# Kernel tuning notes

Measured on AMD Instinct MI355X. Metric: run time of the kernel, lower is better.

The kernel has to match this reference:

```python
import jax, jax.numpy as jnp
import numpy as np

DEPTH = 6
INPUT_DIM = 512
HIDDEN = [128, 64]
OUT_DIM = 8
BATCH = 8192
NUM_LEAVES = 2 ** DEPTH            # 64
NUM_INTERNAL = 2 ** DEPTH - 1      # 63 routing Dense(1, sigmoid) nodes


def setup_inputs() -> dict:
    key = jax.random.key(0)
    ks = jax.random.split(key, 9)
    s = lambda fan_in: 1.0 / np.sqrt(fan_in)
    return {
        "x": jax.random.normal(ks[0], (BATCH, INPUT_DIM), dtype=jnp.float32),
        # routers: one Dense(input_dim -> 1) per internal node
        "router_W": jax.random.normal(ks[1], (NUM_INTERNAL, INPUT_DIM), dtype=jnp.float32) * s(INPUT_DIM),
        "router_b": jnp.zeros((NUM_INTERNAL,), dtype=jnp.float32),
        # leaf MLPs: Dense(512->128, relu) -> Dense(128->64, relu) -> Dense(64->8, linear), one per leaf
        "W1": jax.random.normal(ks[2], (NUM_LEAVES, INPUT_DIM, HIDDEN[0]), dtype=jnp.float32) * s(INPUT_DIM),
        "b1": jnp.zeros((NUM_LEAVES, HIDDEN[0]), dtype=jnp.float32),
        "W2": jax.random.normal(ks[3], (NUM_LEAVES, HIDDEN[0], HIDDEN[1]), dtype=jnp.float32) * s(HIDDEN[0]),
        "b2": jnp.zeros((NUM_LEAVES, HIDDEN[1]), dtype=jnp.float32),
        "W3": jax.random.normal(ks[4], (NUM_LEAVES, HIDDEN[1], OUT_DIM), dtype=jnp.float32) * s(HIDDEN[1]),
        "b3": jnp.zeros((NUM_LEAVES, OUT_DIM), dtype=jnp.float32),
    }


def reference(x, router_W, router_b, W1, b1, W2, b2, W3, b3):
    B = x.shape[0]
    depth = int(np.log2(router_W.shape[0] + 1))
    # All routing probabilities in one fused GEMM: [B, num_internal]
    route = jax.nn.sigmoid(jnp.einsum('bi,ni->bn', x, router_W) + router_b)
    # Soft routing down the tree: interleave left/right child probabilities per level.
    p = jnp.ones((B, 1), dtype=x.dtype)
    offset = 0
    for level in range(depth):  # small fixed loop over tree levels
        n = 2 ** level
        d = route[:, offset:offset + n]              # P(go left) at each node in level
        p = jnp.stack([p * d, p * (1.0 - d)], axis=-1).reshape(B, 2 * n)
        offset += n
    # p: [B, num_leaves] leaf arrival probabilities (sums to 1 per row)
    # Leaf experts as batched (grouped) GEMMs over the leaf axis l.
    h = jax.nn.relu(jnp.einsum('bi,lih->blh', x, W1) + b1)   # [B, L, 128]
    h = jax.nn.relu(jnp.einsum('blh,lhk->blk', h, W2) + b2)  # [B, L, 64]
    pred = jnp.einsum('blk,lko->blo', h, W3) + b3            # [B, L, out] (linear output act)
    # Weighted mixture over leaves.
    return jnp.einsum('bl,blo->bo', p, pred)                 # [B, out]
```

## Files before the change

### kernel.cpp

```cpp
#include <hip/hip_runtime.h>
#include <hip/hip_bf16.h>


typedef _Float16 f16;
typedef _Float16 f16x8 __attribute__((ext_vector_type(8)));
typedef float    f32x4 __attribute__((ext_vector_type(4)));
typedef float    f32x16 __attribute__((ext_vector_type(16)));

#define MFMA16(a,b,c) __builtin_amdgcn_mfma_f32_16x16x32_f16((a),(b),(c),0,0,0)
#define MFMA32(a,b,c) __builtin_amdgcn_mfma_f32_32x32x16_f16((a),(b),(c),0,0,0)

typedef const __attribute__((address_space(1))) void gv_t;
typedef __attribute__((address_space(3))) void lv_t;
__device__ __forceinline__ void cp16(const void* g, char* lds_dst) {
  __builtin_amdgcn_global_load_lds((gv_t*)g, (lv_t*)lds_dst, 16, 0, 0);
}

#define WS_XH    0u
#define WS_W1F   8388608u
#define WS_W2F   16777216u
#define WS_W3F   17825792u
#define WS_RWF   17956864u
#define WS_NEED  18022400u

#define L_X   0
#define L_H1  32768
#define L_H2  41472
#define L_P   46080
#define L_TOT 50176

__global__ __launch_bounds__(256) void prep_all(
    const float* __restrict__ x, const float* __restrict__ rW,
    const float* __restrict__ W1, const float* __restrict__ W2,
    const float* __restrict__ W3,
    f16* __restrict__ xh, f16* __restrict__ w1f, f16* __restrict__ w2f,
    f16* __restrict__ w3f, f16* __restrict__ rwf) {
  __shared__ float sb[8704];
  const int bid = blockIdx.x, t = threadIdx.x;
  if (bid < 512) {
    const int l = bid >> 3, kc = bid & 7;
    const float* src = W1 + ((size_t)l * 512 + kc * 64) * 128;
#pragma unroll
    for (int i = 0; i < 32; ++i) {
      int idx = t + i * 256;
      int k_l = idx >> 7, n = idx & 127;
      sb[n * 68 + k_l] = src[(size_t)k_l * 128 + n];
    }
    __syncthreads();
#pragma unroll
    for (int p = 0; p < 4; ++p) {
      int c = p * 4 + (t >> 6);
      int ng = c >> 2, ksl = c & 3;
      int lane = t & 63;
      int n = ng * 32 + (lane & 31);
      int k0 = ksl * 16 + (lane >> 5) * 8;
      f16x8 h;
#pragma unroll
      for (int j = 0; j < 8; ++j) h[j] = (f16)sb[n * 68 + k0 + j];
      *(f16x8*)(w1f + ((size_t)((l * 4 + ng) * 32 + kc * 4 + ksl) * 64 + lane) * 8) = h;
    }
  } else if (bid < 768) {
    size_t base = (size_t)(bid - 512) * 16384;
#pragma unroll
    for (int i = 0; i < 8; ++i) {
      size_t idx = base + ((size_t)t + i * 256) * 8;
      float4 a = *(const float4*)(x + idx);
      float4 b = *(const float4*)(x + idx + 4);
      f16x8 h = {(f16)a.x,(f16)a.y,(f16)a.z,(f16)a.w,(f16)b.x,(f16)b.y,(f16)b.z,(f16)b.w};
      *(f16x8*)(xh + idx) = h;
    }
  } else if (bid < 832) {
    const int l = bid - 768;
    const float* src = W2 + (size_t)l * 128 * 64;
#pragma unroll
    for (int i = 0; i < 32; ++i) {
      int idx = t + i * 256;
      int k_l = idx >> 6, n = idx & 63;
      sb[n * 132 + k_l] = src[(size_t)k_l * 64 + n];
    }
    __syncthreads();
#pragma unroll
    for (int p = 0; p < 4; ++p) {
      int c = p * 4 + (t >> 6);
      int nb = c >> 2, ks = c & 3;
      int lane = t & 63;
      int n = nb * 16 + (lane & 15);
      int k0 = ks * 32 + (lane >> 4) * 8;
      f16x8 h;
#pragma unroll
      for (int j = 0; j < 8; ++j) h[j] = (f16)sb[n * 132 + k0 + j];
      *(f16x8*)(w2f + ((size_t)((l * 4 + nb) * 4 + ks) * 64 + lane) * 8) = h;
    }
    if (t < 128) {
      int ks = t >> 6, lane = t & 63;
      int n = lane & 15;
      int k0 = ks * 32 + (lane >> 4) * 8;
      f16x8 h;
#pragma unroll
      for (int j = 0; j < 8; ++j)
        h[j] = (n < 8) ? (f16)W3[((size_t)l * 64 + k0 + j) * 8 + n] : (f16)0.f;
      *(f16x8*)(w3f + ((size_t)(l * 2 + ks) * 64 + lane) * 8) = h;
    }
  } else {
    int c = (bid - 832) * 4 + (t >> 6);
    int ngr = c >> 5, ks = c & 31;
    int lane = t & 63;
    int n = ngr * 32 + (lane & 31);
    int k0 = ks * 16 + (lane >> 5) * 8;
    f16x8 h;
#pragma unroll
    for (int j = 0; j < 8; ++j)
      h[j] = (n < 63) ? (f16)rW[(size_t)n * 512 + k0 + j] : (f16)0.f;
    *(f16x8*)(rwf + ((size_t)c * 64 + lane) * 8) = h;
  }
}

__global__ __launch_bounds__(256, 2) void fused_tree(
    const f16* __restrict__ xh, const f16* __restrict__ w1f,
    const f16* __restrict__ w2f, const f16* __restrict__ w3f,
    const f16* __restrict__ rwf, const float* __restrict__ rb,
    const float* __restrict__ b1, const float* __restrict__ b2,
    const float* __restrict__ b3, float* __restrict__ out) {
  __shared__ char smem[L_TOT];
  f16*   x_lds   = (f16*)(smem + L_X);
  f16*   h1_lds  = (f16*)(smem + L_H1);
  float* route_s = (float*)(smem + L_H1);
  f16*   h2_lds  = (f16*)(smem + L_H2);
  float* p_lds   = (float*)(smem + L_P);

  const int t = threadIdx.x;
  const int w = t >> 6, L = t & 63;
  const int l16 = L & 15, quad = L >> 4;
  const int r31 = L & 31, kp = L >> 5;

  const int bid = blockIdx.x;
  const int r8 = bid & 7;
  const int lg0 = (r8 >> 1) * 16;
  const int btp = (bid >> 3) * 2 + (r8 & 1);
  const int b0 = btp * 64;

#pragma unroll
  for (int j = 0; j < 8; ++j) {
    int r = w * 8 + j;
    int u = (L & 56) | ((L & 7) ^ (r & 7));
    cp16(xh + (size_t)(b0 + 32 + r) * 512 + u * 8, smem + r * 1024);
  }
  f16x8 a0[32];
#pragma unroll
  for (int ks = 0; ks < 32; ++ks)
    a0[ks] = *(const f16x8*)(xh + (size_t)(b0 + r31) * 512 + ks * 16 + kp * 8);
  __syncthreads();

  {
    const int btr = w >> 1, ngr = w & 1;
    f32x16 accr;
#pragma unroll
    for (int i = 0; i < 16; ++i) accr[i] = 0.f;
    const f16* rbase = rwf + (size_t)(ngr * 32) * 512 + (size_t)L * 8;
#pragma unroll
    for (int ks = 0; ks < 32; ++ks) {
      f16x8 B = *(const f16x8*)(rbase + (size_t)ks * 512);
      f16x8 A;
      if (btr == 0) A = a0[ks];
      else {
        int u = ks * 2 + kp;
        A = *(const f16x8*)(x_lds + r31 * 512 + ((u & 56) | ((u & 7) ^ (r31 & 7))) * 8);
      }
      accr = MFMA32(A, B, accr);
    }
    int node = ngr * 32 + r31;
    float rbv = (node < 63) ? rb[node] : 0.f;
#pragma unroll
    for (int reg = 0; reg < 16; ++reg) {
      int rr = btr * 32 + (reg & 3) + 8 * (reg >> 2) + 4 * kp;
      route_s[rr * 68 + node] = 1.f / (1.f + __expf(-(accr[reg] + rbv)));
    }
  }
  __syncthreads();
  float prod[4];
  {
    int row = t >> 2, j0 = t & 3;
#pragma unroll
    for (int i = 0; i < 4; ++i) {
      int l = lg0 + j0 * 4 + i;
      float pr = 1.f;
#pragma unroll
      for (int lev = 0; lev < 6; ++lev) {
        int node = (1 << lev) - 1 + (l >> (6 - lev));
        float d = route_s[row * 68 + node];
        pr *= ((l >> (5 - lev)) & 1) ? (1.f - d) : d;
      }
      prod[i] = pr;
    }
  }
  __syncthreads();
  {
    int row = t >> 2, j0 = t & 3;
#pragma unroll
    for (int i = 0; i < 4; ++i) p_lds[row * 16 + j0 * 4 + i] = prod[i];
  }
  __syncthreads();

  const f16* w1base = w1f + ((size_t)(lg0 * 4 + w) * 32) * 512 + (size_t)L * 8;
  f16x8 bq[2][4];
#pragma unroll
  for (int s = 0; s < 4; ++s) bq[0][s] = *(const f16x8*)(w1base + (size_t)s * 512);

  f32x4 acc_out = {0.f, 0.f, 0.f, 0.f};
  const int mt = w >> 1, nt2 = w & 1;

#pragma unroll 1
  for (int li = 0; li < 16; ++li) {
    const int l = lg0 + li;
    const size_t leafoff = (size_t)li * 65536;

    f32x16 acc1r, acc1l;
#pragma unroll
    for (int i = 0; i < 16; ++i) { acc1r[i] = 0.f; acc1l[i] = 0.f; }

#pragma unroll
    for (int q = 0; q < 8; ++q) {
      f16x8 A1[4];
#pragma unroll
      for (int s = 0; s < 4; ++s) {
        int u = (q * 4 + s) * 2 + kp;
        A1[s] = *(const f16x8*)(x_lds + r31 * 512 + ((u & 56) | ((u & 7) ^ (r31 & 7))) * 8);
      }
      size_t nxt = (q < 7) ? (leafoff + (size_t)(q + 1) * 2048)
                           : ((li < 15) ? (leafoff + 65536) : (leafoff + 7 * 2048));
#pragma unroll
      for (int s = 0; s < 4; ++s)
        bq[(q + 1) & 1][s] = *(const f16x8*)(w1base + nxt + (size_t)s * 512);
#pragma unroll
      for (int s = 0; s < 4; ++s)
        acc1r = MFMA32(a0[q * 4 + s], bq[q & 1][s], acc1r);
#pragma unroll
      for (int s = 0; s < 4; ++s)
        acc1l = MFMA32(A1[s], bq[q & 1][s], acc1l);
    }

    f16x8 bw2[2][4];
#pragma unroll
    for (int n16 = 0; n16 < 2; ++n16)
#pragma unroll
      for (int ks = 0; ks < 4; ++ks)
        bw2[n16][ks] = *(const f16x8*)(w2f + ((size_t)((l * 4 + nt2 * 2 + n16) * 4 + ks) * 64 + L) * 8);
    f16x8 bw3[2];
#pragma unroll
    for (int ks = 0; ks < 2; ++ks)
      bw3[ks] = *(const f16x8*)(w3f + ((size_t)(l * 2 + ks) * 64 + L) * 8);

    const int n1 = w * 32 + r31;
    const float bias1 = b1[l * 128 + n1];

#pragma unroll
    for (int reg = 0; reg < 16; ++reg) {
      int rr = (reg & 3) + 8 * (reg >> 2) + 4 * kp;
      float v = acc1r[reg] + bias1;
      h1_lds[rr * 136 + n1] = (f16)(v > 0.f ? v : 0.f);
    }
    __syncthreads();

#define GEMM2_BT(btv)                                                          \
    {                                                                          \
      f32x4 acc2[2] = {{0.f,0.f,0.f,0.f},{0.f,0.f,0.f,0.f}};                   \
      _Pragma("unroll")                                                        \
      for (int ks = 0; ks < 4; ++ks) {                                         \
        f16x8 A = *(const f16x8*)(h1_lds + (mt * 16 + l16) * 136 + ks * 32 + quad * 8); \
        _Pragma("unroll")                                                      \
        for (int n16 = 0; n16 < 2; ++n16) acc2[n16] = MFMA16(A, bw2[n16][ks], acc2[n16]); \
      }                                                                        \
      _Pragma("unroll")                                                        \
      for (int n16 = 0; n16 < 2; ++n16) {                                      \
        int n2 = nt2 * 32 + n16 * 16 + l16;                                    \
        float bias2 = b2[l * 64 + n2];                                         \
        _Pragma("unroll")                                                      \
        for (int rg = 0; rg < 4; ++rg) {                                       \
          int r2 = mt * 16 + quad * 4 + rg;                                    \
          float v = acc2[n16][rg] + bias2;                                     \
          v = v > 0.f ? v : 0.f;                                               \
          h2_lds[r2 * 72 + n2] = (f16)(v * p_lds[((btv) * 32 + r2) * 16 + li]); \
        }                                                                      \
      }                                                                        \
    }

    GEMM2_BT(0)
    __syncthreads();

    if (w < 2) {
#pragma unroll
      for (int ks = 0; ks < 2; ++ks) {
        f16x8 A = *(const f16x8*)(h2_lds + ((w & 1) * 16 + l16) * 72 + ks * 32 + quad * 8);
        acc_out = MFMA16(A, bw3[ks], acc_out);
      }
    }
#pragma unroll
    for (int reg = 0; reg < 16; ++reg) {
      int rr = (reg & 3) + 8 * (reg >> 2) + 4 * kp;
      float v = acc1l[reg] + bias1;
      h1_lds[rr * 136 + n1] = (f16)(v > 0.f ? v : 0.f);
    }
    __syncthreads();

    GEMM2_BT(1)
    __syncthreads();

    if (w >= 2) {
#pragma unroll
      for (int ks = 0; ks < 2; ++ks) {
        f16x8 A = *(const f16x8*)(h2_lds + ((w & 1) * 16 + l16) * 72 + ks * 32 + quad * 8);
        acc_out = MFMA16(A, bw3[ks], acc_out);
      }
    }
#undef GEMM2_BT
  }

  if (l16 < 8) {
    const int btf = w >> 1, mtf = w & 1;
    float b3v[16];
#pragma unroll
    for (int li2 = 0; li2 < 16; ++li2) b3v[li2] = b3[(lg0 + li2) * 8 + l16];
#pragma unroll
    for (int rg = 0; rg < 4; ++rg) {
      int rloc = btf * 32 + mtf * 16 + quad * 4 + rg;
      float v = acc_out[rg];
#pragma unroll
      for (int li2 = 0; li2 < 16; ++li2) v += p_lds[rloc * 16 + li2] * b3v[li2];
      atomicAdd(out + (size_t)(b0 + rloc) * 8 + l16, v);
    }
  }
}

extern "C" void kernel_launch(void* const* d_in, const int* in_sizes, int n_in,
                              void* d_out, int out_size, void* d_ws, size_t ws_size,
                              hipStream_t stream) {
  const float* x  = (const float*)d_in[0];
  const float* rW = (const float*)d_in[1];
  const float* rb = (const float*)d_in[2];
  const float* W1 = (const float*)d_in[3];
  const float* b1 = (const float*)d_in[4];
  const float* W2 = (const float*)d_in[5];
  const float* b2 = (const float*)d_in[6];
  const float* W3 = (const float*)d_in[7];
  const float* b3 = (const float*)d_in[8];
  float* out = (float*)d_out;

  if (ws_size < WS_NEED) return;

  char* ws = (char*)d_ws;
  f16* xh  = (f16*)(ws + WS_XH);
  f16* w1f = (f16*)(ws + WS_W1F);
  f16* w2f = (f16*)(ws + WS_W2F);
  f16* w3f = (f16*)(ws + WS_W3F);
  f16* rwf = (f16*)(ws + WS_RWF);

  hipMemsetAsync(d_out, 0, (size_t)out_size * sizeof(float), stream);
  prep_all<<<848, 256, 0, stream>>>(x, rW, W1, W2, W3, xh, w1f, w2f, w3f, rwf);
  fused_tree<<<512, 256, 0, stream>>>(xh, w1f, w2f, w3f, rwf, rb, b1, b2, b3, out);
}
```

Baseline: 198.2 us.

## Software-pipeline leaf GEMM1 with GEMM2/GEMM3 and double-size h1/h2 buffers

Restructures the per-leaf loop so the layer-1 GEMM for the next leaf is interleaved with the layer-2 and layer-3 work of the current leaf. The h1 and h2 LDS buffers are enlarged to hold both 32-row batch halves at once, which cuts the syncthreads per leaf from four to two. Routing-probability values are preloaded into registers, one barrier in the prologue is removed, and LDS pads in prep and route are changed to odd strides to reduce bank conflicts. The cost is more LDS per block and higher register pressure from the live accumulators, which may lower occupancy.

```diff
diff --git a/kernel.cpp b/kernel.cpp
--- a/kernel.cpp
+++ b/kernel.cpp
@@ -25,9 +25,9 @@
 
 #define L_X   0
 #define L_H1  32768
-#define L_H2  41472
-#define L_P   46080
-#define L_TOT 50176
+#define L_H2  50176
+#define L_P   59392
+#define L_TOT 63488
 
 __global__ __launch_bounds__(256) void prep_all(
     const float* __restrict__ x, const float* __restrict__ rW,
@@ -44,7 +44,7 @@
     for (int i = 0; i < 32; ++i) {
       int idx = t + i * 256;
       int k_l = idx >> 7, n = idx & 127;
-      sb[n * 68 + k_l] = src[(size_t)k_l * 128 + n];
+      sb[n * 65 + k_l] = src[(size_t)k_l * 128 + n];
     }
     __syncthreads();
 #pragma unroll
@@ -56,7 +56,7 @@
       int k0 = ksl * 16 + (lane >> 5) * 8;
       f16x8 h;
 #pragma unroll
-      for (int j = 0; j < 8; ++j) h[j] = (f16)sb[n * 68 + k0 + j];
+      for (int j = 0; j < 8; ++j) h[j] = (f16)sb[n * 65 + k0 + j];
       *(f16x8*)(w1f + ((size_t)((l * 4 + ng) * 32 + kc * 4 + ksl) * 64 + lane) * 8) = h;
     }
   } else if (bid < 768) {
@@ -76,7 +76,7 @@
     for (int i = 0; i < 32; ++i) {
       int idx = t + i * 256;
       int k_l = idx >> 6, n = idx & 63;
-      sb[n * 132 + k_l] = src[(size_t)k_l * 64 + n];
+      sb[n * 129 + k_l] = src[(size_t)k_l * 64 + n];
     }
     __syncthreads();
 #pragma unroll
@@ -88,7 +88,7 @@
       int k0 = ks * 32 + (lane >> 4) * 8;
       f16x8 h;
 #pragma unroll
-      for (int j = 0; j < 8; ++j) h[j] = (f16)sb[n * 132 + k0 + j];
+      for (int j = 0; j < 8; ++j) h[j] = (f16)sb[n * 129 + k0 + j];
       *(f16x8*)(w2f + ((size_t)((l * 4 + nb) * 4 + ks) * 64 + lane) * 8) = h;
     }
     if (t < 128) {
@@ -173,11 +173,10 @@
 #pragma unroll
     for (int reg = 0; reg < 16; ++reg) {
       int rr = btr * 32 + (reg & 3) + 8 * (reg >> 2) + 4 * kp;
-      route_s[rr * 68 + node] = 1.f / (1.f + __expf(-(accr[reg] + rbv)));
+      route_s[rr * 65 + node] = 1.f / (1.f + __expf(-(accr[reg] + rbv)));
     }
   }
   __syncthreads();
-  float prod[4];
   {
     int row = t >> 2, j0 = t & 3;
 #pragma unroll
@@ -187,17 +186,11 @@
 #pragma unroll
       for (int lev = 0; lev < 6; ++lev) {
         int node = (1 << lev) - 1 + (l >> (6 - lev));
-        float d = route_s[row * 68 + node];
+        float d = route_s[row * 65 + node];
         pr *= ((l >> (5 - lev)) & 1) ? (1.f - d) : d;
       }
-      prod[i] = pr;
-    }
-  }
-  __syncthreads();
-  {
-    int row = t >> 2, j0 = t & 3;
-#pragma unroll
-    for (int i = 0; i < 4; ++i) p_lds[row * 16 + j0 * 4 + i] = prod[i];
+      p_lds[row * 16 + j0 * 4 + i] = pr;
+    }
   }
   __syncthreads();
 
@@ -206,67 +199,61 @@
 #pragma unroll
   for (int s = 0; s < 4; ++s) bq[0][s] = *(const f16x8*)(w1base + (size_t)s * 512);
 
+  const int mt = w >> 1, nt2 = w & 1;
+  const int hb = w >> 1;
+  const int n1 = w * 32 + r31;
+
+  f32x16 acc1r, acc1l;
+
+#define G1_STEP(li, q)                                                         \
+    {                                                                          \
+      const size_t leafoff = (size_t)(li) * 65536;                             \
+      f16x8 A1[4];                                                             \
+      _Pragma("unroll")                                                        \
+      for (int s = 0; s < 4; ++s) {                                            \
+        int u = ((q) * 4 + s) * 2 + kp;                                        \
+        A1[s] = *(const f16x8*)(x_lds + r31 * 512 + ((u & 56) | ((u & 7) ^ (r31 & 7))) * 8); \
+      }                                                                        \
+      size_t nxt = ((q) < 7) ? (leafoff + (size_t)((q) + 1) * 2048)            \
+                             : (((li) < 15) ? (leafoff + 65536) : (leafoff + 7 * 2048)); \
+      _Pragma("unroll")                                                        \
+      for (int s = 0; s < 4; ++s)                                              \
+        bq[((q) + 1) & 1][s] = *(const f16x8*)(w1base + nxt + (size_t)s * 512); \
+      _Pragma("unroll")                                                        \
+      for (int s = 0; s < 4; ++s)                                              \
+        acc1r = MFMA32(a0[(q) * 4 + s], bq[(q) & 1][s], acc1r);                \
+      _Pragma("unroll")                                                        \
+      for (int s = 0; s < 4; ++s)                                              \
+        acc1l = MFMA32(A1[s], bq[(q) & 1][s], acc1l);                          \
+    }
+
+#define H1WRITE(lx)                                                            \
+    {                                                                          \
+      const float bias1 = b1[(lx) * 128 + n1];                                 \
+      _Pragma("unroll")                                                        \
+      for (int reg = 0; reg < 16; ++reg) {                                     \
+        int rr = (reg & 3) + 8 * (reg >> 2) + 4 * kp;                          \
+        float v0 = acc1r[reg] + bias1;                                         \
+        float v1 = acc1l[reg] + bias1;                                         \
+        h1_lds[rr * 136 + n1] = (f16)(v0 > 0.f ? v0 : 0.f);                    \
+        h1_lds[(rr + 32) * 136 + n1] = (f16)(v1 > 0.f ? v1 : 0.f);             \
+      }                                                                        \
+    }
+
+#pragma unroll
+  for (int i = 0; i < 16; ++i) { acc1r[i] = 0.f; acc1l[i] = 0.f; }
+#pragma unroll
+  for (int q = 0; q < 8; ++q) G1_STEP(0, q)
+  H1WRITE(0)
+
   f32x4 acc_out = {0.f, 0.f, 0.f, 0.f};
-  const int mt = w >> 1, nt2 = w & 1;
-
-#pragma unroll 1
-  for (int li = 0; li < 16; ++li) {
-    const int l = lg0 + li;
-    const size_t leafoff = (size_t)li * 65536;
-
-    f32x16 acc1r, acc1l;
-#pragma unroll
-    for (int i = 0; i < 16; ++i) { acc1r[i] = 0.f; acc1l[i] = 0.f; }
-
-#pragma unroll
-    for (int q = 0; q < 8; ++q) {
-      f16x8 A1[4];
-#pragma unroll
-      for (int s = 0; s < 4; ++s) {
-        int u = (q * 4 + s) * 2 + kp;
-        A1[s] = *(const f16x8*)(x_lds + r31 * 512 + ((u & 56) | ((u & 7) ^ (r31 & 7))) * 8);
-      }
-      size_t nxt = (q < 7) ? (leafoff + (size_t)(q + 1) * 2048)
-                           : ((li < 15) ? (leafoff + 65536) : (leafoff + 7 * 2048));
-#pragma unroll
-      for (int s = 0; s < 4; ++s)
-        bq[(q + 1) & 1][s] = *(const f16x8*)(w1base + nxt + (size_t)s * 512);
-#pragma unroll
-      for (int s = 0; s < 4; ++s)
-        acc1r = MFMA32(a0[q * 4 + s], bq[q & 1][s], acc1r);
-#pragma unroll
-      for (int s = 0; s < 4; ++s)
-        acc1l = MFMA32(A1[s], bq[q & 1][s], acc1l);
-    }
-
-    f16x8 bw2[2][4];
-#pragma unroll
-    for (int n16 = 0; n16 < 2; ++n16)
-#pragma unroll
-      for (int ks = 0; ks < 4; ++ks)
-        bw2[n16][ks] = *(const f16x8*)(w2f + ((size_t)((l * 4 + nt2 * 2 + n16) * 4 + ks) * 64 + L) * 8);
-    f16x8 bw3[2];
-#pragma unroll
-    for (int ks = 0; ks < 2; ++ks)
-      bw3[ks] = *(const f16x8*)(w3f + ((size_t)(l * 2 + ks) * 64 + L) * 8);
-
-    const int n1 = w * 32 + r31;
-    const float bias1 = b1[l * 128 + n1];
-
-#pragma unroll
-    for (int reg = 0; reg < 16; ++reg) {
-      int rr = (reg & 3) + 8 * (reg >> 2) + 4 * kp;
-      float v = acc1r[reg] + bias1;
-      h1_lds[rr * 136 + n1] = (f16)(v > 0.f ? v : 0.f);
-    }
-    __syncthreads();
 
 #define GEMM2_BT(btv)                                                          \
     {                                                                          \
       f32x4 acc2[2] = {{0.f,0.f,0.f,0.f},{0.f,0.f,0.f,0.f}};                   \
       _Pragma("unroll")                                                        \
       for (int ks = 0; ks < 4; ++ks) {                                         \
-        f16x8 A = *(const f16x8*)(h1_lds + (mt * 16 + l16) * 136 + ks * 32 + quad * 8); \
+        f16x8 A = *(const f16x8*)(h1_lds + ((btv) * 32 + mt * 16 + l16) * 136 + ks * 32 + quad * 8); \
         _Pragma("unroll")                                                      \
         for (int n16 = 0; n16 < 2; ++n16) acc2[n16] = MFMA16(A, bw2[n16][ks], acc2[n16]); \
       }                                                                        \
@@ -279,41 +266,68 @@
           int r2 = mt * 16 + quad * 4 + rg;                                    \
           float v = acc2[n16][rg] + bias2;                                     \
           v = v > 0.f ? v : 0.f;                                               \
-          h2_lds[r2 * 72 + n2] = (f16)(v * p_lds[((btv) * 32 + r2) * 16 + li]); \
+          h2_lds[((btv) * 32 + r2) * 72 + n2] = (f16)(v * pv[btv][rg]);        \
         }                                                                      \
       }                                                                        \
     }
 
+#pragma unroll 1
+  for (int li = 0; li < 16; ++li) {
+    const int l = lg0 + li;
+
+    __syncthreads();
+
+    f16x8 bw2[2][4], bw3[2];
+#pragma unroll
+    for (int n16 = 0; n16 < 2; ++n16)
+#pragma unroll
+      for (int ks = 0; ks < 4; ++ks)
+        bw2[n16][ks] = *(const f16x8*)(w2f + ((size_t)((l * 4 + nt2 * 2 + n16) * 4 + ks) * 64 + L) * 8);
+#pragma unroll
+    for (int ks = 0; ks < 2; ++ks)
+      bw3[ks] = *(const f16x8*)(w3f + ((size_t)(l * 2 + ks) * 64 + L) * 8);
+
+    float pv[2][4];
+#pragma unroll
+    for (int rg = 0; rg < 4; ++rg) {
+      int r2 = mt * 16 + quad * 4 + rg;
+      pv[0][rg] = p_lds[r2 * 16 + li];
+      pv[1][rg] = p_lds[(32 + r2) * 16 + li];
+    }
+
+    if (li < 15) {
+#pragma unroll
+      for (int i = 0; i < 16; ++i) { acc1r[i] = 0.f; acc1l[i] = 0.f; }
+      G1_STEP(li + 1, 0)
+      G1_STEP(li + 1, 1)
+    }
     GEMM2_BT(0)
+    if (li < 15) {
+      G1_STEP(li + 1, 2)
+      G1_STEP(li + 1, 3)
+    }
+    GEMM2_BT(1)
+
     __syncthreads();
 
-    if (w < 2) {
-#pragma unroll
-      for (int ks = 0; ks < 2; ++ks) {
-        f16x8 A = *(const f16x8*)(h2_lds + ((w & 1) * 16 + l16) * 72 + ks * 32 + quad * 8);
-        acc_out = MFMA16(A, bw3[ks], acc_out);
-      }
-    }
-#pragma unroll
-    for (int reg = 0; reg < 16; ++reg) {
-      int rr = (reg & 3) + 8 * (reg >> 2) + 4 * kp;
-      float v = acc1l[reg] + bias1;
-      h1_lds[rr * 136 + n1] = (f16)(v > 0.f ? v : 0.f);
-    }
-    __syncthreads();
-
-    GEMM2_BT(1)
-    __syncthreads();
-
-    if (w >= 2) {
-#pragma unroll
-      for (int ks = 0; ks < 2; ++ks) {
-        f16x8 A = *(const f16x8*)(h2_lds + ((w & 1) * 16 + l16) * 72 + ks * 32 + quad * 8);
-        acc_out = MFMA16(A, bw3[ks], acc_out);
-      }
-    }
+    if (li < 15) {
+      G1_STEP(li + 1, 4)
+      G1_STEP(li + 1, 5)
+    }
+#pragma unroll
+    for (int ks = 0; ks < 2; ++ks) {
+      f16x8 A = *(const f16x8*)(h2_lds + (hb * 32 + (w & 1) * 16 + l16) * 72 + ks * 32 + quad * 8);
+      acc_out = MFMA16(A, bw3[ks], acc_out);
+    }
+    if (li < 15) {
+      G1_STEP(li + 1, 6)
+      G1_STEP(li + 1, 7)
+      H1WRITE(li + 1)
+    }
+  }
 #undef GEMM2_BT
-  }
+#undef G1_STEP
+#undef H1WRITE
 
   if (l16 < 8) {
     const int btf = w >> 1, mtf = w & 1;
```

After: 216.0 us. 9.0% more time.

## Merge both batch-tile GEMM2 passes, swizzle LDS tiles, and raise MFMA priority

Applied to the files above, without the earlier changes.

Each leaf iteration now writes both halves of the layer-1 activations to a doubled h1 buffer and runs GEMM2 for both batch tiles in one pass. This cuts the per-leaf barriers from four to two and removes the idle-half-warps GEMM3 branches, so every warp handles 16 output rows. The h1 and h2 LDS tiles get XOR/rotation swizzles to reduce bank conflicts, prep-kernel transpose pads change to odd strides, and s_setprio brackets the MFMA block. The costs are more LDS per block, which may lower occupancy, and more live registers.

```diff
diff --git a/kernel.cpp b/kernel.cpp
--- a/kernel.cpp
+++ b/kernel.cpp
@@ -25,9 +25,9 @@
 
 #define L_X   0
 #define L_H1  32768
-#define L_H2  41472
-#define L_P   46080
-#define L_TOT 50176
+#define L_H2  50176
+#define L_P   59392
+#define L_TOT 63488
 
 __global__ __launch_bounds__(256) void prep_all(
     const float* __restrict__ x, const float* __restrict__ rW,
@@ -44,7 +44,7 @@
     for (int i = 0; i < 32; ++i) {
       int idx = t + i * 256;
       int k_l = idx >> 7, n = idx & 127;
-      sb[n * 68 + k_l] = src[(size_t)k_l * 128 + n];
+      sb[n * 65 + k_l] = src[(size_t)k_l * 128 + n];
     }
     __syncthreads();
 #pragma unroll
@@ -56,7 +56,7 @@
       int k0 = ksl * 16 + (lane >> 5) * 8;
       f16x8 h;
 #pragma unroll
-      for (int j = 0; j < 8; ++j) h[j] = (f16)sb[n * 68 + k0 + j];
+      for (int j = 0; j < 8; ++j) h[j] = (f16)sb[n * 65 + k0 + j];
       *(f16x8*)(w1f + ((size_t)((l * 4 + ng) * 32 + kc * 4 + ksl) * 64 + lane) * 8) = h;
     }
   } else if (bid < 768) {
@@ -76,7 +76,7 @@
     for (int i = 0; i < 32; ++i) {
       int idx = t + i * 256;
       int k_l = idx >> 6, n = idx & 63;
-      sb[n * 132 + k_l] = src[(size_t)k_l * 64 + n];
+      sb[n * 129 + k_l] = src[(size_t)k_l * 64 + n];
     }
     __syncthreads();
 #pragma unroll
@@ -88,7 +88,7 @@
       int k0 = ks * 32 + (lane >> 4) * 8;
       f16x8 h;
 #pragma unroll
-      for (int j = 0; j < 8; ++j) h[j] = (f16)sb[n * 132 + k0 + j];
+      for (int j = 0; j < 8; ++j) h[j] = (f16)sb[n * 129 + k0 + j];
       *(f16x8*)(w2f + ((size_t)((l * 4 + nb) * 4 + ks) * 64 + lane) * 8) = h;
     }
     if (t < 128) {
@@ -173,11 +173,10 @@
 #pragma unroll
     for (int reg = 0; reg < 16; ++reg) {
       int rr = btr * 32 + (reg & 3) + 8 * (reg >> 2) + 4 * kp;
-      route_s[rr * 68 + node] = 1.f / (1.f + __expf(-(accr[reg] + rbv)));
+      route_s[rr * 65 + node] = 1.f / (1.f + __expf(-(accr[reg] + rbv)));
     }
   }
   __syncthreads();
-  float prod[4];
   {
     int row = t >> 2, j0 = t & 3;
 #pragma unroll
@@ -187,17 +186,11 @@
 #pragma unroll
       for (int lev = 0; lev < 6; ++lev) {
         int node = (1 << lev) - 1 + (l >> (6 - lev));
-        float d = route_s[row * 68 + node];
+        float d = route_s[row * 65 + node];
         pr *= ((l >> (5 - lev)) & 1) ? (1.f - d) : d;
       }
-      prod[i] = pr;
-    }
-  }
-  __syncthreads();
-  {
-    int row = t >> 2, j0 = t & 3;
-#pragma unroll
-    for (int i = 0; i < 4; ++i) p_lds[row * 16 + j0 * 4 + i] = prod[i];
+      p_lds[row * 16 + j0 * 4 + i] = pr;
+    }
   }
   __syncthreads();
 
@@ -208,6 +201,7 @@
 
   f32x4 acc_out = {0.f, 0.f, 0.f, 0.f};
   const int mt = w >> 1, nt2 = w & 1;
+  const int n1 = w * 32 + r31;
 
 #pragma unroll 1
   for (int li = 0; li < 16; ++li) {
@@ -231,12 +225,14 @@
 #pragma unroll
       for (int s = 0; s < 4; ++s)
         bq[(q + 1) & 1][s] = *(const f16x8*)(w1base + nxt + (size_t)s * 512);
+      __builtin_amdgcn_s_setprio(1);
 #pragma unroll
       for (int s = 0; s < 4; ++s)
         acc1r = MFMA32(a0[q * 4 + s], bq[q & 1][s], acc1r);
 #pragma unroll
       for (int s = 0; s < 4; ++s)
         acc1l = MFMA32(A1[s], bq[q & 1][s], acc1l);
+      __builtin_amdgcn_s_setprio(0);
     }
 
     f16x8 bw2[2][4];
@@ -250,79 +246,77 @@
     for (int ks = 0; ks < 2; ++ks)
       bw3[ks] = *(const f16x8*)(w3f + ((size_t)(l * 2 + ks) * 64 + L) * 8);
 
-    const int n1 = w * 32 + r31;
+    float pv[2][4];
+#pragma unroll
+    for (int rg = 0; rg < 4; ++rg) {
+      int r2 = mt * 16 + quad * 4 + rg;
+      pv[0][rg] = p_lds[r2 * 16 + li];
+      pv[1][rg] = p_lds[(32 + r2) * 16 + li];
+    }
+
     const float bias1 = b1[l * 128 + n1];
 
 #pragma unroll
     for (int reg = 0; reg < 16; ++reg) {
       int rr = (reg & 3) + 8 * (reg >> 2) + 4 * kp;
-      float v = acc1r[reg] + bias1;
-      h1_lds[rr * 136 + n1] = (f16)(v > 0.f ? v : 0.f);
+      int c0 = ((((n1 >> 3) + (rr >> 1)) & 15) << 3) | (n1 & 7);
+      float v0 = acc1r[reg] + bias1;
+      float v1 = acc1l[reg] + bias1;
+      h1_lds[rr * 136 + c0] = (f16)(v0 > 0.f ? v0 : 0.f);
+      h1_lds[(rr + 32) * 136 + c0] = (f16)(v1 > 0.f ? v1 : 0.f);
     }
     __syncthreads();
 
-#define GEMM2_BT(btv)                                                          \
-    {                                                                          \
-      f32x4 acc2[2] = {{0.f,0.f,0.f,0.f},{0.f,0.f,0.f,0.f}};                   \
-      _Pragma("unroll")                                                        \
-      for (int ks = 0; ks < 4; ++ks) {                                         \
-        f16x8 A = *(const f16x8*)(h1_lds + (mt * 16 + l16) * 136 + ks * 32 + quad * 8); \
-        _Pragma("unroll")                                                      \
-        for (int n16 = 0; n16 < 2; ++n16) acc2[n16] = MFMA16(A, bw2[n16][ks], acc2[n16]); \
-      }                                                                        \
-      _Pragma("unroll")                                                        \
-      for (int n16 = 0; n16 < 2; ++n16) {                                      \
-        int n2 = nt2 * 32 + n16 * 16 + l16;                                    \
-        float bias2 = b2[l * 64 + n2];                                         \
-        _Pragma("unroll")                                                      \
-        for (int rg = 0; rg < 4; ++rg) {                                       \
-          int r2 = mt * 16 + quad * 4 + rg;                                    \
-          float v = acc2[n16][rg] + bias2;                                     \
-          v = v > 0.f ? v : 0.f;                                               \
-          h2_lds[r2 * 72 + n2] = (f16)(v * p_lds[((btv) * 32 + r2) * 16 + li]); \
-        }                                                                      \
-      }                                                                        \
-    }
-
-    GEMM2_BT(0)
+    f32x4 acc2[2][2] = {{{0.f,0.f,0.f,0.f},{0.f,0.f,0.f,0.f}},
+                        {{0.f,0.f,0.f,0.f},{0.f,0.f,0.f,0.f}}};
+#pragma unroll
+    for (int bt = 0; bt < 2; ++bt) {
+      f16x8 A2[4];
+#pragma unroll
+      for (int ks = 0; ks < 4; ++ks) {
+        int row = bt * 32 + mt * 16 + l16;
+        int cg = (((ks * 4 + quad) + (row >> 1)) & 15) << 3;
+        A2[ks] = *(const f16x8*)(h1_lds + row * 136 + cg);
+      }
+#pragma unroll
+      for (int ks = 0; ks < 4; ++ks)
+#pragma unroll
+        for (int n16 = 0; n16 < 2; ++n16)
+          acc2[bt][n16] = MFMA16(A2[ks], bw2[n16][ks], acc2[bt][n16]);
+    }
+#pragma unroll
+    for (int bt = 0; bt < 2; ++bt)
+#pragma unroll
+      for (int n16 = 0; n16 < 2; ++n16) {
+        int n2 = nt2 * 32 + n16 * 16 + l16;
+        float bias2 = b2[l * 64 + n2];
+#pragma unroll
+        for (int rg = 0; rg < 4; ++rg) {
+          int row = bt * 32 + mt * 16 + quad * 4 + rg;
+          float v = acc2[bt][n16][rg] + bias2;
+          v = v > 0.f ? v : 0.f;
+          int cg = ((((n2 >> 3) + (row >> 1)) & 7) << 3) | (n2 & 7);
+          h2_lds[row * 72 + cg] = (f16)(v * pv[bt][rg]);
+        }
+      }
     __syncthreads();
 
-    if (w < 2) {
-#pragma unroll
-      for (int ks = 0; ks < 2; ++ks) {
-        f16x8 A = *(const f16x8*)(h2_lds + ((w & 1) * 16 + l16) * 72 + ks * 32 + quad * 8);
-        acc_out = MFMA16(A, bw3[ks], acc_out);
-      }
-    }
-#pragma unroll
-    for (int reg = 0; reg < 16; ++reg) {
-      int rr = (reg & 3) + 8 * (reg >> 2) + 4 * kp;
-      float v = acc1l[reg] + bias1;
-      h1_lds[rr * 136 + n1] = (f16)(v > 0.f ? v : 0.f);
-    }
-    __syncthreads();
-
-    GEMM2_BT(1)
-    __syncthreads();
-
-    if (w >= 2) {
-#pragma unroll
-      for (int ks = 0; ks < 2; ++ks) {
-        f16x8 A = *(const f16x8*)(h2_lds + ((w & 1) * 16 + l16) * 72 + ks * 32 + quad * 8);
-        acc_out = MFMA16(A, bw3[ks], acc_out);
-      }
-    }
-#undef GEMM2_BT
+#pragma unroll
+    for (int ks = 0; ks < 2; ++ks) {
+      int row = w * 16 + l16;
+      int cg = (((ks * 4 + quad) + (row >> 1)) & 7) << 3;
+      f16x8 A = *(const f16x8*)(h2_lds + row * 72 + cg);
+      acc_out = MFMA16(A, bw3[ks], acc_out);
+    }
   }
 
   if (l16 < 8) {
-    const int btf = w >> 1, mtf = w & 1;
     float b3v[16];
 #pragma unroll
     for (int li2 = 0; li2 < 16; ++li2) b3v[li2] = b3[(lg0 + li2) * 8 + l16];
 #pragma unroll
     for (int rg = 0; rg < 4; ++rg) {
-      int rloc = btf * 32 + mtf * 16 + quad * 4 + rg;
+      int rloc = w * 16 + quad * 4 + rg;
       float v = acc_out[rg];
 #pragma unroll
       for (int li2 = 0; li2 < 16; ++li2) v += p_lds[rloc * 16 + li2] * b3v[li2];
```

Measured after the change: 223.9 us. 13.0% more time.
